# Performance work log

Measured on AMD Instinct MI355X. Metric: run time of the kernel, lower is better.

## Reference

```python
import jax, jax.numpy as jnp
import numpy as np

CH, HEADS, DH, NMEM, GROUPS, EPS = 128, 4, 32, 4, 32, 1e-5
HID = HEADS * DH

def group_norm(x, w, b):
    # x: [B,C,D,H,W], normalize per group of channels over (C//G, D, H, W)
    B, C = x.shape[0], x.shape[1]
    xg = x.reshape(B, GROUPS, -1)
    mu = xg.mean(axis=-1, keepdims=True)
    var = xg.var(axis=-1, keepdims=True)
    xg = (xg - mu) * jax.lax.rsqrt(var + EPS)
    x = xg.reshape(x.shape)
    return x * w[None, :, None, None, None] + b[None, :, None, None, None]

def setup_inputs() -> dict:
    key = jax.random.key(0)
    ks = jax.random.split(key, 8)
    B, D, H, W = 2, 16, 64, 64
    x = jax.random.normal(ks[0], (B, CH, D, H, W), dtype=jnp.float32)
    norm1_w = jnp.ones((CH,), jnp.float32)
    norm1_b = jnp.zeros((CH,), jnp.float32)
    w_qkv = jax.random.normal(ks[1], (3 * HID, CH), dtype=jnp.float32) * (CH ** -0.5)
    mem_kv = jax.random.normal(ks[2], (2, HEADS, DH, NMEM), dtype=jnp.float32)
    w_out = jax.random.normal(ks[3], (CH, HID), dtype=jnp.float32) * (HID ** -0.5)
    b_out = jnp.zeros((CH,), jnp.float32)
    norm2_w = jnp.ones((CH,), jnp.float32)
    norm2_b = jnp.zeros((CH,), jnp.float32)
    return {"x": x, "norm1_w": norm1_w, "norm1_b": norm1_b, "w_qkv": w_qkv,
            "mem_kv": mem_kv, "w_out": w_out, "b_out": b_out,
            "norm2_w": norm2_w, "norm2_b": norm2_b}

def reference(x, norm1_w, norm1_b, w_qkv, mem_kv, w_out, b_out, norm2_w, norm2_b):
    B, C, D, H, W = x.shape
    n = D * H * W
    scale = DH ** -0.5
    xn = group_norm(x, norm1_w, norm1_b)
    # 1x1x1 conv == channel matmul: [B,3*HID,n]
    qkv = jnp.einsum('oc,bcn->bon', w_qkv, xn.reshape(B, C, n))
    qkv = qkv.reshape(B, 3, HEADS, DH, n)
    q, k, v = qkv[:, 0], qkv[:, 1], qkv[:, 2]  # [B,HEADS,DH,n]
    mk = jnp.broadcast_to(mem_kv[0][None], (B, HEADS, DH, NMEM))
    mv = jnp.broadcast_to(mem_kv[1][None], (B, HEADS, DH, NMEM))
    k = jnp.concatenate([mk, k], axis=-1)
    v = jnp.concatenate([mv, v], axis=-1)
    q = jax.nn.softmax(q, axis=-2) * scale   # over dim_head
    k = jax.nn.softmax(k, axis=-1)           # over sequence
    context = jnp.einsum('bhdn,bhen->bhde', k, v)  # [B,HEADS,DH,DH]
    out = jnp.einsum('bhde,bhdn->bhen', context, q)  # [B,HEADS,DH,n]
    out = out.reshape(B, HID, D, H, W)
    out = jnp.einsum('oc,bcdhw->bodhw', w_out, out) + b_out[None, :, None, None, None]
    return group_norm(out, norm2_w, norm2_b)
```

## Files before the change

### kernel.cpp

```cpp
#include <hip/hip_runtime.h>
#include <math.h>

#define CH     128
#define EPSV   1e-5f
#define SCALE  0.17677669529663687f
#define GSIZE  262144.0f

typedef short bf16x8 __attribute__((ext_vector_type(8)));
typedef short bf16x4 __attribute__((ext_vector_type(4)));
typedef float f32x4  __attribute__((ext_vector_type(4)));

__device__ __forceinline__ unsigned cvtpk(float lo, float hi) {
    unsigned r;
    asm("v_cvt_pk_bf16_f32 %0, %1, %2" : "=v"(r) : "v"(lo), "v"(hi));
    return r;
}
__device__ __forceinline__ bf16x4 pk4(unsigned p01, unsigned p23) {
    union { unsigned u[2]; bf16x4 v; } t;
    t.u[0] = p01; t.u[1] = p23;
    return t.v;
}
__device__ __forceinline__ bf16x8 pk8(unsigned a, unsigned b, unsigned c, unsigned d) {
    union { unsigned u[4]; bf16x8 v; } t;
    t.u[0] = a; t.u[1] = b; t.u[2] = c; t.u[3] = d;
    return t.v;
}
__device__ __forceinline__ unsigned short f2bf(float f) {
    unsigned u = __float_as_uint(f);
    u += 0x7FFF + ((u >> 16) & 1);
    return (unsigned short)(u >> 16);
}
__device__ __forceinline__ float bf2f(unsigned short s) {
    return __uint_as_float(((unsigned)s) << 16);
}

__global__ __launch_bounds__(256) void gn_partial(const float* __restrict__ x,
                                                  float* __restrict__ part) {
    __shared__ float s1[256], s2[256];
    int t = threadIdx.x;
    const float4* xp = (const float4*)(x + (size_t)blockIdx.x * 8192);
    float s = 0.f, q = 0.f;
#pragma unroll
    for (int i = 0; i < 8; ++i) {
        float4 v = xp[t + 256 * i];
        s += v.x + v.y + v.z + v.w;
        q += v.x * v.x + v.y * v.y + v.z * v.z + v.w * v.w;
    }
    s1[t] = s; s2[t] = q;
    __syncthreads();
    for (int st = 128; st > 0; st >>= 1) {
        if (t < st) { s1[t] += s1[t + st]; s2[t] += s2[t + st]; }
        __syncthreads();
    }
    if (t == 0) { part[2 * blockIdx.x] = s1[0]; part[2 * blockIdx.x + 1] = s2[0]; }
}

__global__ void prep1(const float* __restrict__ part, float* __restrict__ mu, float* __restrict__ rs) {
    int t = threadIdx.x;
    float s = 0.f, q = 0.f;
    for (int i = 0; i < 32; ++i) { s += part[2*(t*32+i)]; q += part[2*(t*32+i)+1]; }
    float m = s * (1.f / GSIZE);
    float v = q * (1.f / GSIZE) - m * m;
    mu[t] = m; rs[t] = rsqrtf(v + EPSV);
}

template<bool WX>
__global__ __launch_bounds__(256) void kv_pass(const float* __restrict__ x,
        const float* __restrict__ w_qkv,
        const float* __restrict__ n1w, const float* __restrict__ n1b,
        const float* __restrict__ mu, const float* __restrict__ rs,
        float* __restrict__ part_kv, short* __restrict__ xnb) {
    __shared__ short xk[16*64*8];
    __shared__ short kvstage[8*256*8];
    __shared__ float betas[256];
    int tid = threadIdx.x;
    int l = tid & 63, w = tid >> 6;
    int ncol = l & 15, kg = l >> 4;
    int b = blockIdx.x >> 8;
    int h = w;

    bf16x8 afrag[4][4];
    float bsum[4] = {0.f, 0.f, 0.f, 0.f};
#pragma unroll
    for (int ks = 0; ks < 4; ++ks) {
        float a0[8], b0[8];
#pragma unroll
        for (int j = 0; j < 8; ++j) {
            int c = 8*kg + 32*ks + j;
            int fg = b*32 + (c >> 2);
            float av = rs[fg] * n1w[c];
            a0[j] = av;
            b0[j] = n1b[c] - mu[fg] * av;
        }
#pragma unroll
        for (int rt = 0; rt < 4; ++rt) {
            const float* p = w_qkv + (size_t)(128 + w*64 + 16*rt + ncol)*CH + 8*kg + 32*ks;
            float4 u0 = *(const float4*)p, u1 = *(const float4*)(p + 4);
            float wv[8] = {u0.x,u0.y,u0.z,u0.w,u1.x,u1.y,u1.z,u1.w};
            afrag[rt][ks] = pk8(cvtpk(wv[0]*a0[0], wv[1]*a0[1]), cvtpk(wv[2]*a0[2], wv[3]*a0[3]),
                                cvtpk(wv[4]*a0[4], wv[5]*a0[5]), cvtpk(wv[6]*a0[6], wv[7]*a0[7]));
#pragma unroll
            for (int j = 0; j < 8; ++j) bsum[rt] += wv[j] * b0[j];
        }
    }
#pragma unroll
    for (int rt = 0; rt < 4; ++rt) {
        bsum[rt] += __shfl_xor(bsum[rt], 16);
        bsum[rt] += __shfl_xor(bsum[rt], 32);
    }
    if (kg == 0) {
#pragma unroll
        for (int rt = 0; rt < 4; ++rt) betas[w*64 + 16*rt + ncol] = bsum[rt];
    }

    int nst = (tid & 15) * 4;
    int cst = (tid >> 4) * 8;

    f32x4 cc[2][2];
#pragma unroll
    for (int i = 0; i < 2; ++i)
#pragma unroll
    for (int j = 0; j < 2; ++j)
#pragma unroll
    for (int q = 0; q < 4; ++q) cc[i][j][q] = 0.f;
    float zacc[2] = {0.f, 0.f};

    float4 xv[8];
    {
        int n0 = ((blockIdx.x * 4) << 6) & 65535;
#pragma unroll
        for (int i = 0; i < 8; ++i)
            xv[i] = *(const float4*)(x + ((size_t)(b*CH + cst + i) << 16) + n0 + nst);
        const float* xf = (const float*)xv;
#pragma unroll
        for (int j = 0; j < 4; ++j) {
            int off = ((cst >> 3)*64 + nst + j) * 8;
            bf16x8 v = pk8(cvtpk(xf[0*4+j], xf[1*4+j]), cvtpk(xf[2*4+j], xf[3*4+j]),
                           cvtpk(xf[4*4+j], xf[5*4+j]), cvtpk(xf[6*4+j], xf[7*4+j]));
            *(bf16x8*)&xk[off] = v;
            if (WX) *(bf16x8*)&xnb[(size_t)(blockIdx.x*4) * 8192 + off] = v;
        }
    }

    for (int t4 = 0; t4 < 4; ++t4) {
        __syncthreads();

        f32x4 acc[4][4];
#pragma unroll
        for (int i = 0; i < 4; ++i)
#pragma unroll
        for (int j = 0; j < 4; ++j)
#pragma unroll
        for (int q = 0; q < 4; ++q) acc[i][j][q] = 0.f;

#pragma unroll
        for (int ks = 0; ks < 4; ++ks) {
            bf16x8 bfr[4];
#pragma unroll
            for (int ct = 0; ct < 4; ++ct)
                bfr[ct] = *(bf16x8*)&xk[((4*ks + kg)*64 + 16*ct + ncol) * 8];
#pragma unroll
            for (int rt = 0; rt < 4; ++rt)
#pragma unroll
            for (int ct = 0; ct < 4; ++ct)
                acc[rt][ct] = __builtin_amdgcn_mfma_f32_16x16x32_bf16(
                    afrag[rt][ks], bfr[ct], acc[rt][ct], 0, 0, 0);
        }

#pragma unroll
        for (int rt = 0; rt < 4; ++rt) {
            int lrow0 = w*64 + 16*rt + 4*kg;
            float be0 = betas[lrow0+0], be1 = betas[lrow0+1];
            float be2 = betas[lrow0+2], be3 = betas[lrow0+3];
#pragma unroll
            for (int ct = 0; ct < 4; ++ct) {
                float v0 = acc[rt][ct][0] + be0, v1 = acc[rt][ct][1] + be1;
                float v2 = acc[rt][ct][2] + be2, v3 = acc[rt][ct][3] + be3;
                if (w < 2) { v0 = __expf(v0); v1 = __expf(v1); v2 = __expf(v2); v3 = __expf(v3); }
                unsigned p01 = cvtpk(v0, v1), p23 = cvtpk(v2, v3);
                unsigned short sv[4] = {(unsigned short)p01, (unsigned short)(p01 >> 16),
                                        (unsigned short)p23, (unsigned short)(p23 >> 16)};
                int n = 16*ct + ncol;
#pragma unroll
                for (int q = 0; q < 4; ++q) {
                    int row = lrow0 + q;
                    int byteoff = ((n >> 3)*4096 + row*16 + (n & 7)*2) ^ (((row >> 2) & 3) << 4);
                    *(unsigned short*)((char*)kvstage + byteoff) = sv[q];
                }
            }
        }
        __syncthreads();

        if (t4 < 3) {
            int n0 = ((blockIdx.x * 4 + t4 + 1) << 6) & 65535;
#pragma unroll
            for (int i = 0; i < 8; ++i)
                xv[i] = *(const float4*)(x + ((size_t)(b*CH + cst + i) << 16) + n0 + nst);
        }

#pragma unroll
        for (int ks = 0; ks < 2; ++ks) {
            bf16x8 ak[2], bv[2];
#pragma unroll
            for (int rt = 0; rt < 2; ++rt) {
                int row = h*32 + 16*rt + ncol;
                int byteoff = ((4*ks + kg)*4096 + row*16) ^ (((row >> 2) & 3) << 4);
                ak[rt] = *(bf16x8*)((char*)kvstage + byteoff);
            }
#pragma unroll
            for (int ct = 0; ct < 2; ++ct) {
                int row = 128 + h*32 + 16*ct + ncol;
                int byteoff = ((4*ks + kg)*4096 + row*16) ^ (((row >> 2) & 3) << 4);
                bv[ct] = *(bf16x8*)((char*)kvstage + byteoff);
            }
#pragma unroll
            for (int rt = 0; rt < 2; ++rt)
#pragma unroll
            for (int j = 0; j < 8; ++j) zacc[rt] += bf2f((unsigned short)ak[rt][j]);
#pragma unroll
            for (int rt = 0; rt < 2; ++rt)
#pragma unroll
            for (int ct = 0; ct < 2; ++ct)
                cc[rt][ct] = __builtin_amdgcn_mfma_f32_16x16x32_bf16(
                    ak[rt], bv[ct], cc[rt][ct], 0, 0, 0);
        }

        if (t4 < 3) {
            const float* xf = (const float*)xv;
#pragma unroll
            for (int j = 0; j < 4; ++j) {
                int off = ((cst >> 3)*64 + nst + j) * 8;
                bf16x8 v = pk8(cvtpk(xf[0*4+j], xf[1*4+j]), cvtpk(xf[2*4+j], xf[3*4+j]),
                               cvtpk(xf[4*4+j], xf[5*4+j]), cvtpk(xf[6*4+j], xf[7*4+j]));
                *(bf16x8*)&xk[off] = v;
                if (WX) *(bf16x8*)&xnb[(size_t)(blockIdx.x*4 + t4 + 1) * 8192 + off] = v;
            }
        }
    }

    float* dst = part_kv + (size_t)blockIdx.x * 4224;
#pragma unroll
    for (int rt = 0; rt < 2; ++rt)
#pragma unroll
    for (int ct = 0; ct < 2; ++ct)
#pragma unroll
    for (int q = 0; q < 4; ++q) {
        int d = 16*rt + 4*kg + q;
        int e = 16*ct + ncol;
        dst[h*1024 + d*32 + e] = cc[rt][ct][q];
    }
#pragma unroll
    for (int rt = 0; rt < 2; ++rt) {
        zacc[rt] += __shfl_xor(zacc[rt], 16);
        zacc[rt] += __shfl_xor(zacc[rt], 32);
    }
    if (kg == 0) {
        dst[4096 + h*32 + ncol]      = zacc[0];
        dst[4096 + h*32 + 16 + ncol] = zacc[1];
    }
}

__global__ __launch_bounds__(256) void reduce_ctx(const float* __restrict__ part_kv,
                                                  const float* __restrict__ mem_kv,
                                                  float* __restrict__ ctx, float* __restrict__ Z) {
    int gid = blockIdx.x * 256 + threadIdx.x;
    int oi = gid >> 2, sub = gid & 3;
    int b = oi / 4224;
    int e = oi - b * 4224;
    const float* p = part_kv + (size_t)b * 256 * 4224 + e;
    float s = 0.f;
    for (int i = sub; i < 256; i += 4) s += p[(size_t)i * 4224];
    s += __shfl_xor(s, 1);
    s += __shfl_xor(s, 2);
    if (sub == 0) {
        if (e < 4096) {
            int hh = e >> 10, d = (e >> 5) & 31, ee = e & 31;
            float init = 0.f;
            for (int m = 0; m < 4; ++m)
                init += expf(mem_kv[hh*128 + d*4 + m]) * mem_kv[512 + hh*128 + ee*4 + m];
            ctx[b*4096 + e] = init + s;
        } else {
            int d2 = e - 4096;
            float init = 0.f;
            for (int m = 0; m < 4; ++m) init += expf(mem_kv[d2*4 + m]);
            Z[b*128 + d2] = init + s;
        }
    }
}

template<bool BF16OUT, bool XNB>
__global__ __launch_bounds__(256) void out_pass(const float* __restrict__ x,
        const short* __restrict__ xnb,
        const float* __restrict__ w_qkv,
        const float* __restrict__ n1w, const float* __restrict__ n1b,
        const float* __restrict__ mu, const float* __restrict__ rs,
        const float* __restrict__ ctx, const float* __restrict__ Z,
        const float* __restrict__ w_out, const float* __restrict__ b_out,
        float* __restrict__ out, unsigned short* __restrict__ outb,
        float* __restrict__ part2) {
    __shared__ short xk[16*64*8];
    __shared__ short pb[16*64*8];
    __shared__ float betasq[128];
    int tid = threadIdx.x;
    int l = tid & 63, w = tid >> 6;
    int ncol = l & 15, kg = l >> 4;
    int b = blockIdx.x >> 8;

    bf16x8 aq[2][4], aw[2][4];
    float bsq[2] = {0.f, 0.f};
#pragma unroll
    for (int ks = 0; ks < 4; ++ks) {
        float a0[8], b0[8];
#pragma unroll
        for (int j = 0; j < 8; ++j) {
            int c = 8*kg + 32*ks + j;
            int fg = b*32 + (c >> 2);
            float av = rs[fg] * n1w[c];
            a0[j] = av;
            b0[j] = n1b[c] - mu[fg] * av;
        }
#pragma unroll
        for (int rt = 0; rt < 2; ++rt) {
            const float* pq = w_qkv + (size_t)(32*w + 16*rt + ncol)*CH + 8*kg + 32*ks;
            const float* pw = w_out + (size_t)(32*w + 16*rt + ncol)*CH + 8*kg + 32*ks;
            float4 u0 = *(const float4*)pq, u1 = *(const float4*)(pq + 4);
            float4 v0 = *(const float4*)pw, v1 = *(const float4*)(pw + 4);
            float wq[8] = {u0.x,u0.y,u0.z,u0.w,u1.x,u1.y,u1.z,u1.w};
            float wo[8] = {v0.x,v0.y,v0.z,v0.w,v1.x,v1.y,v1.z,v1.w};
            aq[rt][ks] = pk8(cvtpk(wq[0]*a0[0], wq[1]*a0[1]), cvtpk(wq[2]*a0[2], wq[3]*a0[3]),
                             cvtpk(wq[4]*a0[4], wq[5]*a0[5]), cvtpk(wq[6]*a0[6], wq[7]*a0[7]));
            aw[rt][ks] = pk8(cvtpk(wo[0], wo[1]), cvtpk(wo[2], wo[3]),
                             cvtpk(wo[4], wo[5]), cvtpk(wo[6], wo[7]));
#pragma unroll
            for (int j = 0; j < 8; ++j) bsq[rt] += wq[j] * b0[j];
        }
    }
#pragma unroll
    for (int rt = 0; rt < 2; ++rt) {
        bsq[rt] += __shfl_xor(bsq[rt], 16);
        bsq[rt] += __shfl_xor(bsq[rt], 32);
    }
    if (kg == 0) {
#pragma unroll
        for (int rt = 0; rt < 2; ++rt) betasq[32*w + 16*rt + ncol] = bsq[rt];
    }

    bf16x8 actx[2];
#pragma unroll
    for (int rt = 0; rt < 2; ++rt) {
        bf16x8 f;
#pragma unroll
        for (int j = 0; j < 8; ++j) {
            int d = 8*kg + j;
            float cv = ctx[b*4096 + w*1024 + d*32 + 16*rt + ncol] / Z[b*128 + w*32 + d];
            f[j] = (short)f2bf(cv);
        }
        actx[rt] = f;
    }

    float bo[2][4];
#pragma unroll
    for (int rt = 0; rt < 2; ++rt)
#pragma unroll
    for (int q = 0; q < 4; ++q)
        bo[rt][q] = b_out[32*w + 16*rt + 4*kg + q];

    int nst = (tid & 15) * 4;
    int cst = (tid >> 4) * 8;
    float pgs[2] = {0.f, 0.f}, pgq[2] = {0.f, 0.f};
    float4 xv[8];
    bf16x8 xr[4];

    {
        if (XNB) {
            const bf16x8* src = (const bf16x8*)(xnb + (size_t)(blockIdx.x*4) * 8192);
#pragma unroll
            for (int j = 0; j < 4; ++j) {
                int fi = (cst >> 3)*64 + nst + j;
                *(bf16x8*)&xk[fi * 8] = src[fi];
            }
        } else {
            int n0 = (blockIdx.x << 8) & 65535;
#pragma unroll
            for (int i = 0; i < 8; ++i)
                xv[i] = *(const float4*)(x + ((size_t)(b*CH + cst + i) << 16) + n0 + nst);
            const float* xf = (const float*)xv;
#pragma unroll
            for (int j = 0; j < 4; ++j)
                *(bf16x8*)&xk[((cst >> 3)*64 + nst + j) * 8] =
                    pk8(cvtpk(xf[0*4+j], xf[1*4+j]), cvtpk(xf[2*4+j], xf[3*4+j]),
                        cvtpk(xf[4*4+j], xf[5*4+j]), cvtpk(xf[6*4+j], xf[7*4+j]));
        }
    }

    for (int t4 = 0; t4 < 4; ++t4) {
        int n0 = ((blockIdx.x*4 + t4) << 6) & 65535;
        __syncthreads();

        f32x4 acc[2][4];
#pragma unroll
        for (int i = 0; i < 2; ++i)
#pragma unroll
        for (int j = 0; j < 4; ++j)
#pragma unroll
        for (int q = 0; q < 4; ++q) acc[i][j][q] = 0.f;
#pragma unroll
        for (int ks = 0; ks < 4; ++ks) {
            bf16x8 bfr[4];
#pragma unroll
            for (int ct = 0; ct < 4; ++ct)
                bfr[ct] = *(bf16x8*)&xk[((4*ks + kg)*64 + 16*ct + ncol) * 8];
#pragma unroll
            for (int rt = 0; rt < 2; ++rt)
#pragma unroll
            for (int ct = 0; ct < 4; ++ct)
                acc[rt][ct] = __builtin_amdgcn_mfma_f32_16x16x32_bf16(
                    aq[rt][ks], bfr[ct], acc[rt][ct], 0, 0, 0);
        }

        {
            float be[2][4];
#pragma unroll
            for (int rt = 0; rt < 2; ++rt)
#pragma unroll
            for (int q = 0; q < 4; ++q) be[rt][q] = betasq[32*w + 16*rt + 4*kg + q];
            float sum[4];
#pragma unroll
            for (int ct = 0; ct < 4; ++ct) {
                float s = 0.f;
#pragma unroll
                for (int rt = 0; rt < 2; ++rt)
#pragma unroll
                for (int q = 0; q < 4; ++q) {
                    float e = __expf(acc[rt][ct][q] + be[rt][q]);
                    acc[rt][ct][q] = e;
                    s += e;
                }
                s += __shfl_xor(s, 16);
                s += __shfl_xor(s, 32);
                sum[ct] = SCALE / s;
            }
#pragma unroll
            for (int ct = 0; ct < 4; ++ct)
#pragma unroll
            for (int rt = 0; rt < 2; ++rt) {
                unsigned p01 = cvtpk(acc[rt][ct][0]*sum[ct], acc[rt][ct][1]*sum[ct]);
                unsigned p23 = cvtpk(acc[rt][ct][2]*sum[ct], acc[rt][ct][3]*sum[ct]);
                int row0 = w*32 + 16*rt + 4*kg;
                *(bf16x4*)&pb[((row0 >> 3)*64 + 16*ct + ncol)*8 + (row0 & 7)] = pk4(p01, p23);
            }
        }

        f32x4 hacc[2][4];
#pragma unroll
        for (int i = 0; i < 2; ++i)
#pragma unroll
        for (int j = 0; j < 4; ++j)
#pragma unroll
        for (int q = 0; q < 4; ++q) hacc[i][j][q] = 0.f;
        {
            bf16x8 bq[4];
#pragma unroll
            for (int ct = 0; ct < 4; ++ct)
                bq[ct] = *(bf16x8*)&pb[((w*4 + kg)*64 + 16*ct + ncol) * 8];
#pragma unroll
            for (int rt = 0; rt < 2; ++rt)
#pragma unroll
            for (int ct = 0; ct < 4; ++ct)
                hacc[rt][ct] = __builtin_amdgcn_mfma_f32_16x16x32_bf16(
                    actx[rt], bq[ct], hacc[rt][ct], 0, 0, 0);
        }

#pragma unroll
        for (int ct = 0; ct < 4; ++ct)
#pragma unroll
        for (int rt = 0; rt < 2; ++rt) {
            unsigned p01 = cvtpk(hacc[rt][ct][0], hacc[rt][ct][1]);
            unsigned p23 = cvtpk(hacc[rt][ct][2], hacc[rt][ct][3]);
            int row0 = w*32 + 16*rt + 4*kg;
            *(bf16x4*)&pb[((row0 >> 3)*64 + 16*ct + ncol)*8 + (row0 & 7)] = pk4(p01, p23);
        }
        __syncthreads();

        if (t4 < 3) {
            if (XNB) {
                const bf16x8* src = (const bf16x8*)(xnb + (size_t)(blockIdx.x*4 + t4 + 1) * 8192);
#pragma unroll
                for (int j = 0; j < 4; ++j)
                    xr[j] = src[(cst >> 3)*64 + nst + j];
            } else {
                int n1 = ((blockIdx.x*4 + t4 + 1) << 6) & 65535;
#pragma unroll
                for (int i = 0; i < 8; ++i)
                    xv[i] = *(const float4*)(x + ((size_t)(b*CH + cst + i) << 16) + n1 + nst);
            }
        }

        f32x4 oacc[2][4];
#pragma unroll
        for (int i = 0; i < 2; ++i)
#pragma unroll
        for (int j = 0; j < 4; ++j)
#pragma unroll
        for (int q = 0; q < 4; ++q) oacc[i][j][q] = 0.f;
#pragma unroll
        for (int ks = 0; ks < 4; ++ks) {
            bf16x8 bfr[4];
#pragma unroll
            for (int ct = 0; ct < 4; ++ct)
                bfr[ct] = *(bf16x8*)&pb[((4*ks + kg)*64 + 16*ct + ncol) * 8];
#pragma unroll
            for (int rt = 0; rt < 2; ++rt)
#pragma unroll
            for (int ct = 0; ct < 4; ++ct)
                oacc[rt][ct] = __builtin_amdgcn_mfma_f32_16x16x32_bf16(
                    aw[rt][ks], bfr[ct], oacc[rt][ct], 0, 0, 0);
        }

#pragma unroll
        for (int rt = 0; rt < 2; ++rt)
#pragma unroll
        for (int ct = 0; ct < 4; ++ct)
#pragma unroll
        for (int q = 0; q < 4; ++q) {
            int c = 32*w + 16*rt + 4*kg + q;
            float o = oacc[rt][ct][q] + bo[rt][q];
            size_t idx = ((size_t)(b*CH + c) << 16) + n0 + 16*ct + ncol;
            if (BF16OUT) outb[idx] = f2bf(o);
            else         out[idx] = o;
            pgs[rt] += o;
            pgq[rt] += o*o;
        }

        if (t4 < 3) {
            if (XNB) {
#pragma unroll
                for (int j = 0; j < 4; ++j)
                    *(bf16x8*)&xk[((cst >> 3)*64 + nst + j) * 8] = xr[j];
            } else {
                const float* xf = (const float*)xv;
#pragma unroll
                for (int j = 0; j < 4; ++j)
                    *(bf16x8*)&xk[((cst >> 3)*64 + nst + j) * 8] =
                        pk8(cvtpk(xf[0*4+j], xf[1*4+j]), cvtpk(xf[2*4+j], xf[3*4+j]),
                            cvtpk(xf[4*4+j], xf[5*4+j]), cvtpk(xf[6*4+j], xf[7*4+j]));
            }
        }
    }

#pragma unroll
    for (int rt = 0; rt < 2; ++rt) {
        float gs = pgs[rt], gq = pgq[rt];
#pragma unroll
        for (int m = 1; m < 16; m <<= 1) {
            gs += __shfl_xor(gs, m);
            gq += __shfl_xor(gq, m);
        }
        if (ncol == 0) {
            int g = 8*w + 4*rt + kg;
            part2[blockIdx.x*64 + g*2 + 0] = gs;
            part2[blockIdx.x*64 + g*2 + 1] = gq;
        }
    }
}

__global__ __launch_bounds__(256) void reduce2(const float* __restrict__ part2,
                                               float* __restrict__ mu, float* __restrict__ rs) {
    __shared__ float s1[256], s2[256];
    int fg = blockIdx.x;
    int b = fg >> 5, g = fg & 31;
    int t = threadIdx.x;
    const float* p = part2 + ((size_t)(b*256 + t))*64 + g*2;
    s1[t] = p[0]; s2[t] = p[1];
    __syncthreads();
    for (int st = 128; st > 0; st >>= 1) {
        if (t < st) { s1[t] += s1[t + st]; s2[t] += s2[t + st]; }
        __syncthreads();
    }
    if (t == 0) {
        float m = s1[0] * (1.f / GSIZE);
        float v = s2[0] * (1.f / GSIZE) - m*m;
        mu[fg] = m; rs[fg] = rsqrtf(v + EPSV);
    }
}

__global__ __launch_bounds__(256) void gn_apply(float* __restrict__ y,
        const float* __restrict__ mu, const float* __restrict__ rs,
        const float* __restrict__ w2, const float* __restrict__ b2) {
    int bi = blockIdx.x, t = threadIdx.x;
    int c = (bi >> 3) & 127;
    int b = bi >> 10;
    int fg = b*32 + (c >> 2);
    float aa = rs[fg] * w2[c];
    float bb = b2[c] - mu[fg] * aa;
    float4* yp = (float4*)(y + (size_t)bi * 8192);
#pragma unroll
    for (int i = 0; i < 8; ++i) {
        float4 v = yp[t + 256*i];
        v.x = v.x*aa+bb; v.y = v.y*aa+bb; v.z = v.z*aa+bb; v.w = v.w*aa+bb;
        yp[t + 256*i] = v;
    }
}

__global__ __launch_bounds__(256) void gn_apply_bf16(const unsigned short* __restrict__ src,
        float* __restrict__ y,
        const float* __restrict__ mu, const float* __restrict__ rs,
        const float* __restrict__ w2, const float* __restrict__ b2) {
    int bi = blockIdx.x, t = threadIdx.x;
    int c = (bi >> 3) & 127;
    int b = bi >> 10;
    int fg = b*32 + (c >> 2);
    float aa = rs[fg] * w2[c];
    float bb = b2[c] - mu[fg] * aa;
    const ushort4* sp = (const ushort4*)(src + (size_t)bi * 8192);
    float4* yp = (float4*)(y + (size_t)bi * 8192);
#pragma unroll
    for (int i = 0; i < 8; ++i) {
        ushort4 u = sp[t + 256*i];
        float4 v;
        v.x = bf2f(u.x)*aa+bb; v.y = bf2f(u.y)*aa+bb;
        v.z = bf2f(u.z)*aa+bb; v.w = bf2f(u.w)*aa+bb;
        yp[t + 256*i] = v;
    }
}

extern "C" void kernel_launch(void* const* d_in, const int* in_sizes, int n_in,
                              void* d_out, int out_size, void* d_ws, size_t ws_size,
                              hipStream_t stream) {
    (void)in_sizes; (void)n_in; (void)out_size;
    const float* x      = (const float*)d_in[0];
    const float* n1w    = (const float*)d_in[1];
    const float* n1b    = (const float*)d_in[2];
    const float* w_qkv  = (const float*)d_in[3];
    const float* mem_kv = (const float*)d_in[4];
    const float* w_out  = (const float*)d_in[5];
    const float* b_out  = (const float*)d_in[6];
    const float* n2w    = (const float*)d_in[7];
    const float* n2b    = (const float*)d_in[8];
    float* out = (float*)d_out;
    float* ws  = (float*)d_ws;

    float* part1   = ws;
    float* mu1     = ws + 4096;
    float* rs1     = ws + 4160;
    float* ctx     = ws + 4224;
    float* Z       = ws + 12416;
    float* part2   = ws + 12672;
    float* mu2     = ws + 143744;
    float* rs2     = ws + 143808;
    float* part_kv = ws + 143872;
    const size_t base_floats = 143872 + (size_t)512*4224;
    unsigned short* outb = (unsigned short*)(ws + base_floats);
    const size_t outb_floats = (size_t)CH*65536;
    short* xnb = (short*)(ws + base_floats + outb_floats);
    const size_t need1 = (base_floats + outb_floats) * 4;
    const size_t need2 = (base_floats + 2*outb_floats) * 4;
    int tier = (ws_size >= need2) ? 2 : (ws_size >= need1 ? 1 : 0);

    gn_partial<<<2048, 256, 0, stream>>>(x, part1);
    prep1<<<1, 64, 0, stream>>>(part1, mu1, rs1);
    if (tier == 2) kv_pass<true><<<512, 256, 0, stream>>>(x, w_qkv, n1w, n1b, mu1, rs1, part_kv, xnb);
    else           kv_pass<false><<<512, 256, 0, stream>>>(x, w_qkv, n1w, n1b, mu1, rs1, part_kv, xnb);
    reduce_ctx<<<132, 256, 0, stream>>>(part_kv, mem_kv, ctx, Z);
    if (tier == 2) {
        out_pass<true,true><<<512, 256, 0, stream>>>(x, xnb, w_qkv, n1w, n1b, mu1, rs1, ctx, Z,
                                                     w_out, b_out, out, outb, part2);
        reduce2<<<64, 256, 0, stream>>>(part2, mu2, rs2);
        gn_apply_bf16<<<2048, 256, 0, stream>>>(outb, out, mu2, rs2, n2w, n2b);
    } else if (tier == 1) {
        out_pass<true,false><<<512, 256, 0, stream>>>(x, xnb, w_qkv, n1w, n1b, mu1, rs1, ctx, Z,
                                                      w_out, b_out, out, outb, part2);
        reduce2<<<64, 256, 0, stream>>>(part2, mu2, rs2);
        gn_apply_bf16<<<2048, 256, 0, stream>>>(outb, out, mu2, rs2, n2w, n2b);
    } else {
        out_pass<false,false><<<512, 256, 0, stream>>>(x, xnb, w_qkv, n1w, n1b, mu1, rs1, ctx, Z,
                                                       w_out, b_out, out, outb, part2);
        reduce2<<<64, 256, 0, stream>>>(part2, mu2, rs2);
        gn_apply<<<2048, 256, 0, stream>>>(out, mu2, rs2, n2w, n2b);
    }
}
```

Before: 121.6 us.

## Fuse GroupNorm stats with bf16 conversion so kv_pass reads bf16 x

```diff
diff --git a/kernel.cpp b/kernel.cpp
--- a/kernel.cpp
+++ b/kernel.cpp
@@ -32,6 +32,76 @@
 }
 __device__ __forceinline__ float bf2f(unsigned short s) {
     return __uint_as_float(((unsigned)s) << 16);
+}
+
+__global__ __launch_bounds__(256) void gn_cvt(const float* __restrict__ x,
+                                              float* __restrict__ part1,
+                                              short* __restrict__ xnb) {
+    int bi = blockIdx.x;
+    int b = bi >> 10;
+    int n0 = (bi & 1023) * 64;
+    int t = threadIdx.x;
+    int nst = (t & 15) * 4;
+    int cst = (t >> 4) * 8;
+
+    float4 xv[8];
+#pragma unroll
+    for (int i = 0; i < 8; ++i)
+        xv[i] = *(const float4*)(x + ((size_t)(b*CH + cst + i) << 16) + n0 + nst);
+    const float* xf = (const float*)xv;
+
+    float s0 = 0.f, q0 = 0.f, s1 = 0.f, q1 = 0.f;
+#pragma unroll
+    for (int i = 0; i < 8; ++i)
+#pragma unroll
+    for (int j = 0; j < 4; ++j) {
+        float v = xf[i*4 + j];
+        if (i < 4) { s0 += v; q0 += v*v; }
+        else       { s1 += v; q1 += v*v; }
+    }
+
+#pragma unroll
+    for (int j = 0; j < 4; ++j)
+        *(bf16x8*)&xnb[(size_t)bi * 8192 + ((cst >> 3)*64 + nst + j) * 8] =
+            pk8(cvtpk(xf[0*4+j], xf[1*4+j]), cvtpk(xf[2*4+j], xf[3*4+j]),
+                cvtpk(xf[4*4+j], xf[5*4+j]), cvtpk(xf[6*4+j], xf[7*4+j]));
+
+#pragma unroll
+    for (int m = 1; m < 16; m <<= 1) {
+        s0 += __shfl_xor(s0, m); q0 += __shfl_xor(q0, m);
+        s1 += __shfl_xor(s1, m); q1 += __shfl_xor(q1, m);
+    }
+    if ((t & 15) == 0) {
+        int g = cst >> 2;
+        part1[bi*64 + g*2 + 0] = s0;
+        part1[bi*64 + g*2 + 1] = q0;
+        part1[bi*64 + (g+1)*2 + 0] = s1;
+        part1[bi*64 + (g+1)*2 + 1] = q1;
+    }
+}
+
+__global__ __launch_bounds__(256) void reduce1(const float* __restrict__ part1,
+                                               float* __restrict__ mu, float* __restrict__ rs) {
+    __shared__ float s1[256], s2[256];
+    int fg = blockIdx.x;
+    int b = fg >> 5, g = fg & 31;
+    int t = threadIdx.x;
+    float s = 0.f, q = 0.f;
+    for (int i = t; i < 1024; i += 256) {
+        const float* p = part1 + ((size_t)(b*1024 + i))*64 + g*2;
+        s += p[0]; q += p[1];
+    }
+    s1[t] = s; s2[t] = q;
+    __syncthreads();
+    for (int st = 128; st > 0; st >>= 1) {
+        if (t < st) { s1[t] += s1[t + st]; s2[t] += s2[t + st]; }
+        __syncthreads();
+    }
+    if (t == 0) {
+        float m = s1[0] * (1.f / GSIZE);
+        float v = s2[0] * (1.f / GSIZE) - m*m;
+        mu[fg] = m; rs[fg] = rsqrtf(v + EPSV);
+    }
 }
 
 __global__ __launch_bounds__(256) void gn_partial(const float* __restrict__ x,
@@ -54,7 +124,6 @@
     }
     if (t == 0) { part[2 * blockIdx.x] = s1[0]; part[2 * blockIdx.x + 1] = s2[0]; }
 }
-
 __global__ void prep1(const float* __restrict__ part, float* __restrict__ mu, float* __restrict__ rs) {
     int t = threadIdx.x;
     float s = 0.f, q = 0.f;
@@ -64,12 +133,13 @@
     mu[t] = m; rs[t] = rsqrtf(v + EPSV);
 }
 
-template<bool WX>
+template<bool XNB>
 __global__ __launch_bounds__(256) void kv_pass(const float* __restrict__ x,
+        const short* __restrict__ xnb,
         const float* __restrict__ w_qkv,
         const float* __restrict__ n1w, const float* __restrict__ n1b,
         const float* __restrict__ mu, const float* __restrict__ rs,
-        float* __restrict__ part_kv, short* __restrict__ xnb) {
+        float* __restrict__ part_kv) {
     __shared__ short xk[16*64*8];
     __shared__ short kvstage[8*256*8];
     __shared__ float betas[256];
@@ -126,19 +196,26 @@
     float zacc[2] = {0.f, 0.f};
 
     float4 xv[8];
+    bf16x8 xr[4];
     {
-        int n0 = ((blockIdx.x * 4) << 6) & 65535;
-#pragma unroll
-        for (int i = 0; i < 8; ++i)
-            xv[i] = *(const float4*)(x + ((size_t)(b*CH + cst + i) << 16) + n0 + nst);
-        const float* xf = (const float*)xv;
-#pragma unroll
-        for (int j = 0; j < 4; ++j) {
-            int off = ((cst >> 3)*64 + nst + j) * 8;
-            bf16x8 v = pk8(cvtpk(xf[0*4+j], xf[1*4+j]), cvtpk(xf[2*4+j], xf[3*4+j]),
-                           cvtpk(xf[4*4+j], xf[5*4+j]), cvtpk(xf[6*4+j], xf[7*4+j]));
-            *(bf16x8*)&xk[off] = v;
-            if (WX) *(bf16x8*)&xnb[(size_t)(blockIdx.x*4) * 8192 + off] = v;
+        if (XNB) {
+            const bf16x8* src = (const bf16x8*)(xnb + (size_t)(blockIdx.x*4) * 8192);
+#pragma unroll
+            for (int j = 0; j < 4; ++j) {
+                int fi = (cst >> 3)*64 + nst + j;
+                *(bf16x8*)&xk[fi * 8] = src[fi];
+            }
+        } else {
+            int n0 = ((blockIdx.x * 4) << 6) & 65535;
+#pragma unroll
+            for (int i = 0; i < 8; ++i)
+                xv[i] = *(const float4*)(x + ((size_t)(b*CH + cst + i) << 16) + n0 + nst);
+            const float* xf = (const float*)xv;
+#pragma unroll
+            for (int j = 0; j < 4; ++j)
+                *(bf16x8*)&xk[((cst >> 3)*64 + nst + j) * 8] =
+                    pk8(cvtpk(xf[0*4+j], xf[1*4+j]), cvtpk(xf[2*4+j], xf[3*4+j]),
+                        cvtpk(xf[4*4+j], xf[5*4+j]), cvtpk(xf[6*4+j], xf[7*4+j]));
         }
     }
 
@@ -192,10 +269,17 @@
         __syncthreads();
 
         if (t4 < 3) {
-            int n0 = ((blockIdx.x * 4 + t4 + 1) << 6) & 65535;
-#pragma unroll
-            for (int i = 0; i < 8; ++i)
-                xv[i] = *(const float4*)(x + ((size_t)(b*CH + cst + i) << 16) + n0 + nst);
+            if (XNB) {
+                const bf16x8* src = (const bf16x8*)(xnb + (size_t)(blockIdx.x*4 + t4 + 1) * 8192);
+#pragma unroll
+                for (int j = 0; j < 4; ++j)
+                    xr[j] = src[(cst >> 3)*64 + nst + j];
+            } else {
+                int n0 = ((blockIdx.x * 4 + t4 + 1) << 6) & 65535;
+#pragma unroll
+                for (int i = 0; i < 8; ++i)
+                    xv[i] = *(const float4*)(x + ((size_t)(b*CH + cst + i) << 16) + n0 + nst);
+            }
         }
 
 #pragma unroll
@@ -226,14 +310,17 @@
         }
 
         if (t4 < 3) {
-            const float* xf = (const float*)xv;
-#pragma unroll
-            for (int j = 0; j < 4; ++j) {
-                int off = ((cst >> 3)*64 + nst + j) * 8;
-                bf16x8 v = pk8(cvtpk(xf[0*4+j], xf[1*4+j]), cvtpk(xf[2*4+j], xf[3*4+j]),
-                               cvtpk(xf[4*4+j], xf[5*4+j]), cvtpk(xf[6*4+j], xf[7*4+j]));
-                *(bf16x8*)&xk[off] = v;
-                if (WX) *(bf16x8*)&xnb[(size_t)(blockIdx.x*4 + t4 + 1) * 8192 + off] = v;
+            if (XNB) {
+#pragma unroll
+                for (int j = 0; j < 4; ++j)
+                    *(bf16x8*)&xk[((cst >> 3)*64 + nst + j) * 8] = xr[j];
+            } else {
+                const float* xf = (const float*)xv;
+#pragma unroll
+                for (int j = 0; j < 4; ++j)
+                    *(bf16x8*)&xk[((cst >> 3)*64 + nst + j) * 8] =
+                        pk8(cvtpk(xf[0*4+j], xf[1*4+j]), cvtpk(xf[2*4+j], xf[3*4+j]),
+                            cvtpk(xf[4*4+j], xf[5*4+j]), cvtpk(xf[6*4+j], xf[7*4+j]));
             }
         }
     }
@@ -477,7 +564,7 @@
         for (int rt = 0; rt < 2; ++rt) {
             unsigned p01 = cvtpk(hacc[rt][ct][0], hacc[rt][ct][1]);
             unsigned p23 = cvtpk(hacc[rt][ct][2], hacc[rt][ct][3]);
-            int row0 = w*32 + 16*rt + 4*kg;
+            int row0 = 32*w + 16*rt + 4*kg;
             *(bf16x4*)&pb[((row0 >> 3)*64 + 16*ct + ncol)*8 + (row0 & 7)] = pk4(p01, p23);
         }
         __syncthreads();
@@ -641,38 +728,45 @@
     float* ws  = (float*)d_ws;
 
     float* part1   = ws;
-    float* mu1     = ws + 4096;
-    float* rs1     = ws + 4160;
-    float* ctx     = ws + 4224;
-    float* Z       = ws + 12416;
-    float* part2   = ws + 12672;
-    float* mu2     = ws + 143744;
-    float* rs2     = ws + 143808;
-    float* part_kv = ws + 143872;
-    const size_t base_floats = 143872 + (size_t)512*4224;
+    float* mu1     = ws + 131072;
+    float* rs1     = ws + 131136;
+    float* ctx     = ws + 131200;
+    float* Z       = ws + 139392;
+    float* part2   = ws + 139648;
+    float* mu2     = ws + 172416;
+    float* rs2     = ws + 172480;
+    float* part_kv = ws + 172544;
+    const size_t base_floats = 172544 + (size_t)512*4224;
     unsigned short* outb = (unsigned short*)(ws + base_floats);
-    const size_t outb_floats = (size_t)CH*65536;
-    short* xnb = (short*)(ws + base_floats + outb_floats);
-    const size_t need1 = (base_floats + outb_floats) * 4;
-    const size_t need2 = (base_floats + 2*outb_floats) * 4;
+    const size_t buf_floats = (size_t)CH*65536;
+    short* xnb = (short*)(ws + base_floats + buf_floats);
+    const size_t need1 = (base_floats + buf_floats) * 4;
+    const size_t need2 = (base_floats + 2*buf_floats) * 4;
     int tier = (ws_size >= need2) ? 2 : (ws_size >= need1 ? 1 : 0);
 
-    gn_partial<<<2048, 256, 0, stream>>>(x, part1);
-    prep1<<<1, 64, 0, stream>>>(part1, mu1, rs1);
-    if (tier == 2) kv_pass<true><<<512, 256, 0, stream>>>(x, w_qkv, n1w, n1b, mu1, rs1, part_kv, xnb);
-    else           kv_pass<false><<<512, 256, 0, stream>>>(x, w_qkv, n1w, n1b, mu1, rs1, part_kv, xnb);
-    reduce_ctx<<<132, 256, 0, stream>>>(part_kv, mem_kv, ctx, Z);
     if (tier == 2) {
+        gn_cvt<<<2048, 256, 0, stream>>>(x, part1, xnb);
+        reduce1<<<64, 256, 0, stream>>>(part1, mu1, rs1);
+        kv_pass<true><<<512, 256, 0, stream>>>(x, xnb, w_qkv, n1w, n1b, mu1, rs1, part_kv);
+        reduce_ctx<<<132, 256, 0, stream>>>(part_kv, mem_kv, ctx, Z);
         out_pass<true,true><<<512, 256, 0, stream>>>(x, xnb, w_qkv, n1w, n1b, mu1, rs1, ctx, Z,
                                                      w_out, b_out, out, outb, part2);
         reduce2<<<64, 256, 0, stream>>>(part2, mu2, rs2);
         gn_apply_bf16<<<2048, 256, 0, stream>>>(outb, out, mu2, rs2, n2w, n2b);
     } else if (tier == 1) {
+        gn_partial<<<2048, 256, 0, stream>>>(x, part1);
+        prep1<<<1, 64, 0, stream>>>(part1, mu1, rs1);
+        kv_pass<false><<<512, 256, 0, stream>>>(x, xnb, w_qkv, n1w, n1b, mu1, rs1, part_kv);
+        reduce_ctx<<<132, 256, 0, stream>>>(part_kv, mem_kv, ctx, Z);
         out_pass<true,false><<<512, 256, 0, stream>>>(x, xnb, w_qkv, n1w, n1b, mu1, rs1, ctx, Z,
                                                       w_out, b_out, out, outb, part2);
         reduce2<<<64, 256, 0, stream>>>(part2, mu2, rs2);
         gn_apply_bf16<<<2048, 256, 0, stream>>>(outb, out, mu2, rs2, n2w, n2b);
     } else {
+        gn_partial<<<2048, 256, 0, stream>>>(x, part1);
+        prep1<<<1, 64, 0, stream>>>(part1, mu1, rs1);
+        kv_pass<false><<<512, 256, 0, stream>>>(x, xnb, w_qkv, n1w, n1b, mu1, rs1, part_kv);
+        reduce_ctx<<<132, 256, 0, stream>>>(part_kv, mem_kv, ctx, Z);
         out_pass<false,false><<<512, 256, 0, stream>>>(x, xnb, w_qkv, n1w, n1b, mu1, rs1, ctx, Z,
                                                        w_out, b_out, out, outb, part2);
         reduce2<<<64, 256, 0, stream>>>(part2, mu2, rs2);
```

After: 124.7 us. +2.6%, slower.
